# Kernel tuning notes

Hardware: AMD Instinct MI355X
Metric: run time of the kernel (lower is better)

Reference implementation:

```python
import jax, jax.numpy as jnp
import numpy as np

T = 0.1  # temperature (init arg t)


def setup_inputs() -> dict:
    key = jax.random.key(0)
    k0, k1, k2, k3 = jax.random.split(key, 4)
    B, C, H, W, N = 1, 64, 256, 256, 4096
    emb_0 = jax.random.normal(k0, (B, C, H, W), dtype=jnp.float32)
    emb_1 = jax.random.normal(k1, (B, C, H, W), dtype=jnp.float32)
    # module assumes embeddings are already L2-normalized along channels
    emb_0 = emb_0 / jnp.linalg.norm(emb_0, axis=1, keepdims=True)
    emb_1 = emb_1 / jnp.linalg.norm(emb_1, axis=1, keepdims=True)
    locations_0 = jax.random.randint(k2, (B, N, 2), 0, H).astype(jnp.float32)
    locations_1 = jax.random.randint(k3, (B, N, 2), 0, H).astype(jnp.float32)
    return {"emb_0": emb_0, "emb_1": emb_1,
            "locations_0": locations_0, "locations_1": locations_1}


def reference(emb_0, emb_1, locations_0, locations_1):
    b, c, H, W = emb_0.shape  # b == 1
    n = locations_0.shape[1]
    v = H * W
    # (b, v, c)
    e0 = emb_0.reshape(b, c, v).transpose(0, 2, 1)
    e1 = emb_1.reshape(b, c, v).transpose(0, 2, 1)
    # flatten 2D coords to linear indices: strides [W, 1]
    ind_kernel = jnp.array([W, 1], dtype=jnp.float32)
    ind_0 = (jnp.floor(locations_0) @ ind_kernel).astype(jnp.int32)[0]  # (n,)
    ind_1 = (jnp.floor(locations_1) @ ind_kernel).astype(jnp.int32)[0]  # (n,)
    e0 = e0[:, ind_0, :]  # (b, n, c)
    e1 = e1[:, ind_1, :]  # (b, n, c)
    emb = jnp.concatenate([e0, e1], axis=1)  # (b, 2n, c)
    sim = jnp.einsum('bic,bjc->bij', emb, emb)  # (b, 2n, 2n)
    exp = jnp.exp(sim / T)
    sum_e = jnp.sum(exp, axis=2) - np.exp(1.0 / T)  # subtract self-similarity
    u = jnp.arange(n)
    w = u + n
    e_uv = exp[:, u, w]  # (b, n) positive pairs
    loss = -jnp.sum(jnp.log(e_uv / sum_e[:, u]) + jnp.log(e_uv / sum_e[:, w]))
    return loss / (2 * n)
```

## Files before the change

kernel.cpp:

```cpp
#include <hip/hip_runtime.h>
#include <math.h>

#define HW2     65536
#define NLOC    4096
#define NROW    8192
#define CDIM    64
#define TINV    10.0f
#define EXP10   22026.465794806718f
#define NP      64
#define NPAIR   2080

#if __has_builtin(__builtin_amdgcn_exp2f)
#define ASCALE  14.426950408889634f
#define EXPFN(x) __builtin_amdgcn_exp2f(x)
#else
#define ASCALE  10.0f
#define EXPFN(x) __expf(x)
#endif

typedef __attribute__((ext_vector_type(8))) short bf16x8;
typedef __attribute__((ext_vector_type(4))) float f32x4;
typedef unsigned short u16;

__device__ __forceinline__ unsigned short f2bf(float f) {
  unsigned u = __builtin_bit_cast(unsigned, f);
  u += 0x7FFFu + ((u >> 16) & 1u);
  return (unsigned short)(u >> 16);
}
__device__ __forceinline__ float bf2f(unsigned u16v) {
  unsigned u = u16v << 16;
  return __builtin_bit_cast(float, u);
}

__global__ __launch_bounds__(256) void tgather_kernel(
    const float* __restrict__ emb0, const float* __restrict__ emb1,
    const float* __restrict__ loc0, const float* __restrict__ loc1,
    u16* __restrict__ Ga, u16* __restrict__ Gb) {
  __shared__ u16 T[64 * 72];
  __shared__ unsigned list[NLOC];
  __shared__ unsigned nE;

  const int tid = threadIdx.x;
  const int win = blockIdx.x;
  const int eb  = blockIdx.y;
  const float* emb = eb ? emb1 : emb0;
  const float* loc = eb ? loc1 : loc0;
  const int w0 = win * 64;

  if (tid == 0) nE = 0;

#pragma unroll
  for (int q = 0; q < 4; ++q) {
    const int c = q * 16 + (tid >> 4);
    const int x = tid & 15;
    float4 v = *reinterpret_cast<const float4*>(&emb[(size_t)c * HW2 + w0 + x * 4]);
    T[(x * 4 + 0) * 72 + c] = f2bf(v.x);
    T[(x * 4 + 1) * 72 + c] = f2bf(v.y);
    T[(x * 4 + 2) * 72 + c] = f2bf(v.z);
    T[(x * 4 + 3) * 72 + c] = f2bf(v.w);
  }
  __syncthreads();

  for (int it = tid; it < NLOC; it += 256) {
    float2 lv = *reinterpret_cast<const float2*>(&loc[it * 2]);
    int ind = (int)floorf(lv.x) * 256 + (int)floorf(lv.y);
    if ((ind >> 6) == win) {
      unsigned slot = atomicAdd(&nE, 1u);
      list[slot] = ((unsigned)it << 6) | (unsigned)(ind & 63);
    }
  }
  __syncthreads();

  const int n = (int)nE;
  const int ibase = eb * NLOC;
  const int c8 = tid & 7;
  for (int s = (tid >> 3); s < n; s += 32) {
    const unsigned ent = list[s];
    const int i = (int)(ent >> 6) + ibase;
    const int w = (int)(ent & 63u);
    bf16x8 v = *reinterpret_cast<const bf16x8*>(&T[w * 72 + c8 * 8]);
    *reinterpret_cast<bf16x8*>(&Gb[(size_t)i * CDIM + c8 * 8]) = v;
    bf16x8 vs;
#pragma unroll
    for (int j = 0; j < 8; ++j) {
      float f = bf2f((unsigned short)v[j]);
      vs[j] = (short)f2bf(f * ASCALE);
    }
    *reinterpret_cast<bf16x8*>(&Ga[(size_t)i * CDIM + c8 * 8]) = vs;
  }
}

__global__ __launch_bounds__(256) void gather_kernel(
    const float* __restrict__ emb0, const float* __restrict__ emb1,
    const float* __restrict__ loc0, const float* __restrict__ loc1,
    u16* __restrict__ Ga, u16* __restrict__ Gb) {
  int t = blockIdx.x * 256 + threadIdx.x;
  int i = t >> 6;
  int c = t & 63;
  const float* loc = (i < NLOC) ? loc0 : loc1;
  const float* emb = (i < NLOC) ? emb0 : emb1;
  int u = (i < NLOC) ? i : (i - NLOC);
  int ind = (int)floorf(loc[u * 2]) * 256 + (int)floorf(loc[u * 2 + 1]);
  float v = emb[(size_t)c * HW2 + ind];
  Gb[t] = f2bf(v);
  Ga[t] = f2bf(v * ASCALE);
}

__device__ __forceinline__ void stage_tile(u16* Bs, const u16* __restrict__ Gb,
                                           int jb, int buf, int tid, int wave,
                                           int srow, int ssl) {
#pragma unroll
  for (int r = 0; r < 2; ++r) {
    const u16* src = Gb + (size_t)(jb + r * 32 + srow) * CDIM + ssl * 8;
#if __has_builtin(__builtin_amdgcn_global_load_lds)
    u16* dst = Bs + buf * 4096 + r * 2048 + wave * 512;
    __builtin_amdgcn_global_load_lds(
        (const __attribute__((address_space(1))) unsigned int*)src,
        (__attribute__((address_space(3))) unsigned int*)dst, 16, 0, 0);
#else
    bf16x8 tmp = *reinterpret_cast<const bf16x8*>(src);
    *reinterpret_cast<bf16x8*>(Bs + buf * 4096 + r * 2048 + tid * 8) = tmp;
#endif
  }
}

__global__ __launch_bounds__(256) void simsum_tri_kernel(
    const u16* __restrict__ Ga, const u16* __restrict__ Gb,
    float* __restrict__ rowPart) {
  __shared__ u16 Bs[2 * 64 * CDIM];
  __shared__ float colRed[4][128];

  const int tid  = threadIdx.x;
  const int lane = tid & 63;
  const int wave = tid >> 6;
  const int lrow = lane & 15;
  const int kh   = lane >> 4;

  const int b = blockIdx.x;
  int p = (int)((129.0f - sqrtf(16641.0f - 8.0f * (float)b)) * 0.5f);
  if (p < 0) p = 0;
  if (p > NP - 1) p = NP - 1;
#pragma unroll
  for (int it = 0; it < 3; ++it) {
    if (p > 0 && (p * NP - p * (p - 1) / 2) > b) --p;
    else if (((p + 1) * NP - (p + 1) * p / 2) <= b) ++p;
  }
  const int q  = p + (b - (p * NP - p * (p - 1) / 2));
  const int p0 = p * 128, q0 = q * 128;
  const int i0 = p0 + wave * 32;

  const bf16x8* arowA =
      reinterpret_cast<const bf16x8*>(Ga + (size_t)(i0 + lrow) * CDIM + kh * 8);
  const bf16x8* arowB =
      reinterpret_cast<const bf16x8*>(Ga + (size_t)(i0 + 16 + lrow) * CDIM + kh * 8);
  bf16x8 aA0 = arowA[0], aA1 = arowA[4];
  bf16x8 aB0 = arowB[0], aB1 = arowB[4];

  const int srow = tid >> 3;
  const int ssl  = (tid & 7) ^ (srow & 7);
  stage_tile(Bs, Gb, q0,      0, tid, wave, srow, ssl);
  stage_tile(Bs, Gb, q0 + 64, 1, tid, wave, srow, ssl);
  __syncthreads();

  const int sp0 = ((kh ^ (lrow & 7)) << 3);
  const int sp1 = (((4 + kh) ^ (lrow & 7)) << 3);

  float accA[4][4], accB[4][4];
#pragma unroll
  for (int nf = 0; nf < 4; ++nf)
#pragma unroll
    for (int r = 0; r < 4; ++r) { accA[nf][r] = 0.f; accB[nf][r] = 0.f; }
  float colAcc[2][4];

#pragma unroll
  for (int t = 0; t < 2; ++t) {
    const u16* bs = Bs + t * 4096;
#pragma unroll
    for (int nf = 0; nf < 4; ++nf) {
      const int rb = (nf * 16 + lrow) * CDIM;
      bf16x8 b0 = *reinterpret_cast<const bf16x8*>(bs + rb + sp0);
      bf16x8 b1 = *reinterpret_cast<const bf16x8*>(bs + rb + sp1);
      f32x4 z = {0.f, 0.f, 0.f, 0.f};
      f32x4 tA = __builtin_amdgcn_mfma_f32_16x16x32_bf16(aA0, b0, z, 0, 0, 0);
      tA = __builtin_amdgcn_mfma_f32_16x16x32_bf16(aA1, b1, tA, 0, 0, 0);
      f32x4 tB = __builtin_amdgcn_mfma_f32_16x16x32_bf16(aB0, b0, z, 0, 0, 0);
      tB = __builtin_amdgcn_mfma_f32_16x16x32_bf16(aB1, b1, tB, 0, 0, 0);
      float cp = 0.f;
#pragma unroll
      for (int r = 0; r < 4; ++r) {
        float eA = EXPFN(tA[r]);
        float eB = EXPFN(tB[r]);
        accA[nf][r] += eA;
        accB[nf][r] += eB;
        cp += eA + eB;
      }
      colAcc[t][nf] = cp;
    }
  }

#pragma unroll
  for (int r = 0; r < 4; ++r) {
    float vA = (accA[0][r] + accA[1][r]) + (accA[2][r] + accA[3][r]);
    float vB = (accB[0][r] + accB[1][r]) + (accB[2][r] + accB[3][r]);
    vA += __shfl_xor(vA, 1, 16);
    vA += __shfl_xor(vA, 2, 16);
    vA += __shfl_xor(vA, 4, 16);
    vA += __shfl_xor(vA, 8, 16);
    vB += __shfl_xor(vB, 1, 16);
    vB += __shfl_xor(vB, 2, 16);
    vB += __shfl_xor(vB, 4, 16);
    vB += __shfl_xor(vB, 8, 16);
    if (lrow == 0) {
      rowPart[(size_t)(i0 + kh * 4 + r) * NP + q] = vA;
      rowPart[(size_t)(i0 + 16 + kh * 4 + r) * NP + q] = vB;
    }
  }

  if (p != q) {
#pragma unroll
    for (int t = 0; t < 2; ++t)
#pragma unroll
      for (int nf = 0; nf < 4; ++nf) {
        float c = colAcc[t][nf];
        c += __shfl_xor(c, 16, 64);
        c += __shfl_xor(c, 32, 64);
        if (kh == 0) colRed[wave][t * 64 + nf * 16 + lrow] = c;
      }
    __syncthreads();
    if (tid < 128) {
      float s = (colRed[0][tid] + colRed[1][tid]) +
                (colRed[2][tid] + colRed[3][tid]);
      rowPart[(size_t)(q0 + tid) * NP + p] = s;
    }
  }
}

__global__ __launch_bounds__(256) void finpart_kernel(
    const u16* __restrict__ Gb, const float* __restrict__ rowPart,
    float* __restrict__ partA, float* __restrict__ partB) {
  __shared__ float sA[256];
  __shared__ float sB[256];
  const int tid = threadIdx.x, b = blockIdx.x;

  float logAcc = 0.f;
  if (tid < 128) {
    const int row = b * 128 + tid;
    const float4* rp = reinterpret_cast<const float4*>(rowPart + (size_t)row * NP);
    float s = 0.f;
#pragma unroll
    for (int c = 0; c < NP / 4; ++c) {
      float4 v = rp[c];
      s += (v.x + v.y) + (v.z + v.w);
    }
    logAcc = logf(s - EXP10);
  }
  float cross = 0.f;
  if (tid < 64) {
    const int u = b * 64 + tid;
    const unsigned* r0 = reinterpret_cast<const unsigned*>(Gb + (size_t)u * CDIM);
    const unsigned* r1 =
        reinterpret_cast<const unsigned*>(Gb + (size_t)(u + NLOC) * CDIM);
#pragma unroll
    for (int c = 0; c < 32; ++c) {
      unsigned a = r0[c], bb = r1[c];
      cross += bf2f(a & 0xffffu) * bf2f(bb & 0xffffu) + bf2f(a >> 16) * bf2f(bb >> 16);
    }
  }
  sA[tid] = logAcc;
  sB[tid] = cross;
  __syncthreads();
  for (int s = 128; s > 0; s >>= 1) {
    if (tid < s) { sA[tid] += sA[tid + s]; sB[tid] += sB[tid + s]; }
    __syncthreads();
  }
  if (tid == 0) { partA[b] = sA[0]; partB[b] = sB[0]; }
}

__global__ __launch_bounds__(64) void fin2_kernel(
    const float* __restrict__ partA, const float* __restrict__ partB,
    float* __restrict__ out) {
  const int l = threadIdx.x;
  float a = partA[l];
  float c = partB[l];
#pragma unroll
  for (int s = 1; s < 64; s <<= 1) {
    a += __shfl_xor(a, s, 64);
    c += __shfl_xor(c, s, 64);
  }
  if (l == 0) out[0] = (a - 2.0f * TINV * c) / (float)NROW;
}

extern "C" void kernel_launch(void* const* d_in, const int* in_sizes, int n_in,
                              void* d_out, int out_size, void* d_ws, size_t ws_size,
                              hipStream_t stream) {
  const float* emb0 = (const float*)d_in[0];
  const float* emb1 = (const float*)d_in[1];
  const float* loc0 = (const float*)d_in[2];
  const float* loc1 = (const float*)d_in[3];
  float* out = (float*)d_out;
  char* ws = (char*)d_ws;

  u16* Ga        = (u16*)ws;
  u16* Gb        = (u16*)(ws + (1ull << 20));
  float* rowPart = (float*)(ws + (2ull << 20));
  float* partA   = (float*)(ws + (4ull << 20));
  float* partB   = partA + 64;

  dim3 tg(HW2 / 64, 2);
  tgather_kernel<<<tg, 256, 0, stream>>>(emb0, emb1, loc0, loc1, Ga, Gb);

  simsum_tri_kernel<<<NPAIR, 256, 0, stream>>>(Ga, Gb, rowPart);
  finpart_kernel<<<64, 256, 0, stream>>>(Gb, rowPart, partA, partB);
  fin2_kernel<<<1, 64, 0, stream>>>(partA, partB, out);
}
```

Before: 41.46 us.

## Replace full-tensor transpose gather with direct point gather and fuse final reduction

The gather stage no longer streams the whole embedding tensors through shared memory. Instead each block reads only the sampled locations for a 16-channel group, stages them in shared memory, and writes coalesced bf16 rows. This is meant to cut the bulk DRAM traffic of reading both full embeddings. The final two-level reduction is folded into finpart using an atomic counter and a last-block pattern, which removes one kernel launch. The trade-off is scattered, sector-granular reads and a little atomic/fence overhead.

```diff
diff --git a/kernel.cpp b/kernel.cpp
--- a/kernel.cpp
+++ b/kernel.cpp
@@ -32,78 +32,55 @@
   return __builtin_bit_cast(float, u);
 }
 
-__global__ __launch_bounds__(256) void tgather_kernel(
+__global__ __launch_bounds__(256) void gatherc_kernel(
     const float* __restrict__ emb0, const float* __restrict__ emb1,
     const float* __restrict__ loc0, const float* __restrict__ loc1,
-    u16* __restrict__ Ga, u16* __restrict__ Gb) {
-  __shared__ u16 T[64 * 72];
-  __shared__ unsigned list[NLOC];
-  __shared__ unsigned nE;
-
-  const int tid = threadIdx.x;
-  const int win = blockIdx.x;
-  const int eb  = blockIdx.y;
+    u16* __restrict__ Ga, u16* __restrict__ Gb, unsigned* __restrict__ counter) {
+  __shared__ int ind[64];
+  __shared__ u16 Gs[64][18];
+
+  const int tid   = threadIdx.x;
+  const int chunk = blockIdx.x;
+  const int cg    = blockIdx.y;
+  const int eb    = chunk >> 6;
   const float* emb = eb ? emb1 : emb0;
   const float* loc = eb ? loc1 : loc0;
-  const int w0 = win * 64;
-
-  if (tid == 0) nE = 0;
-
-#pragma unroll
-  for (int q = 0; q < 4; ++q) {
-    const int c = q * 16 + (tid >> 4);
-    const int x = tid & 15;
-    float4 v = *reinterpret_cast<const float4*>(&emb[(size_t)c * HW2 + w0 + x * 4]);
-    T[(x * 4 + 0) * 72 + c] = f2bf(v.x);
-    T[(x * 4 + 1) * 72 + c] = f2bf(v.y);
-    T[(x * 4 + 2) * 72 + c] = f2bf(v.z);
-    T[(x * 4 + 3) * 72 + c] = f2bf(v.w);
-  }
-  __syncthreads();
-
-  for (int it = tid; it < NLOC; it += 256) {
-    float2 lv = *reinterpret_cast<const float2*>(&loc[it * 2]);
-    int ind = (int)floorf(lv.x) * 256 + (int)floorf(lv.y);
-    if ((ind >> 6) == win) {
-      unsigned slot = atomicAdd(&nE, 1u);
-      list[slot] = ((unsigned)it << 6) | (unsigned)(ind & 63);
-    }
-  }
-  __syncthreads();
-
-  const int n = (int)nE;
-  const int ibase = eb * NLOC;
-  const int c8 = tid & 7;
-  for (int s = (tid >> 3); s < n; s += 32) {
-    const unsigned ent = list[s];
-    const int i = (int)(ent >> 6) + ibase;
-    const int w = (int)(ent & 63u);
-    bf16x8 v = *reinterpret_cast<const bf16x8*>(&T[w * 72 + c8 * 8]);
-    *reinterpret_cast<bf16x8*>(&Gb[(size_t)i * CDIM + c8 * 8]) = v;
+
+  if (chunk == 0 && cg == 0 && tid == 0) *counter = 0u;
+
+  if (tid < 64) {
+    const int u = (chunk & 63) * 64 + tid;
+    float2 lv = *reinterpret_cast<const float2*>(&loc[u * 2]);
+    ind[tid] = (int)floorf(lv.x) * 256 + (int)floorf(lv.y);
+  }
+  __syncthreads();
+
+  const int row = tid & 63;
+  const int cq  = tid >> 6;
+  const int pos = ind[row];
+#pragma unroll
+  for (int k = 0; k < 4; ++k) {
+    const int cl = cq + 4 * k;
+    float v = emb[(size_t)(cg * 16 + cl) * HW2 + pos];
+    Gs[row][cl] = f2bf(v);
+  }
+  __syncthreads();
+
+  const int t  = tid & 127;
+  const int r2 = t >> 1, h = t & 1;
+  const size_t gi = (size_t)(chunk * 64 + r2) * CDIM + cg * 16 + h * 8;
+  bf16x8 v = *reinterpret_cast<const bf16x8*>(&Gs[r2][h * 8]);
+  if (tid < 128) {
+    *reinterpret_cast<bf16x8*>(&Gb[gi]) = v;
+  } else {
     bf16x8 vs;
 #pragma unroll
     for (int j = 0; j < 8; ++j) {
       float f = bf2f((unsigned short)v[j]);
       vs[j] = (short)f2bf(f * ASCALE);
     }
-    *reinterpret_cast<bf16x8*>(&Ga[(size_t)i * CDIM + c8 * 8]) = vs;
-  }
-}
-
-__global__ __launch_bounds__(256) void gather_kernel(
-    const float* __restrict__ emb0, const float* __restrict__ emb1,
-    const float* __restrict__ loc0, const float* __restrict__ loc1,
-    u16* __restrict__ Ga, u16* __restrict__ Gb) {
-  int t = blockIdx.x * 256 + threadIdx.x;
-  int i = t >> 6;
-  int c = t & 63;
-  const float* loc = (i < NLOC) ? loc0 : loc1;
-  const float* emb = (i < NLOC) ? emb0 : emb1;
-  int u = (i < NLOC) ? i : (i - NLOC);
-  int ind = (int)floorf(loc[u * 2]) * 256 + (int)floorf(loc[u * 2 + 1]);
-  float v = emb[(size_t)c * HW2 + ind];
-  Gb[t] = f2bf(v);
-  Ga[t] = f2bf(v * ASCALE);
+    *reinterpret_cast<bf16x8*>(&Ga[gi]) = vs;
+  }
 }
 
 __device__ __forceinline__ void stage_tile(u16* Bs, const u16* __restrict__ Gb,
@@ -237,9 +214,11 @@
 
 __global__ __launch_bounds__(256) void finpart_kernel(
     const u16* __restrict__ Gb, const float* __restrict__ rowPart,
-    float* __restrict__ partA, float* __restrict__ partB) {
+    float* __restrict__ partA, float* __restrict__ partB,
+    unsigned* __restrict__ counter, float* __restrict__ out) {
   __shared__ float sA[256];
   __shared__ float sB[256];
+  __shared__ int lastFlag;
   const int tid = threadIdx.x, b = blockIdx.x;
 
   float logAcc = 0.f;
@@ -273,21 +252,25 @@
     if (tid < s) { sA[tid] += sA[tid + s]; sB[tid] += sB[tid + s]; }
     __syncthreads();
   }
-  if (tid == 0) { partA[b] = sA[0]; partB[b] = sB[0]; }
-}
-
-__global__ __launch_bounds__(64) void fin2_kernel(
-    const float* __restrict__ partA, const float* __restrict__ partB,
-    float* __restrict__ out) {
-  const int l = threadIdx.x;
-  float a = partA[l];
-  float c = partB[l];
-#pragma unroll
-  for (int s = 1; s < 64; s <<= 1) {
-    a += __shfl_xor(a, s, 64);
-    c += __shfl_xor(c, s, 64);
-  }
-  if (l == 0) out[0] = (a - 2.0f * TINV * c) / (float)NROW;
+  if (tid == 0) {
+    __hip_atomic_store(&partA[b], sA[0], __ATOMIC_RELAXED, __HIP_MEMORY_SCOPE_AGENT);
+    __hip_atomic_store(&partB[b], sB[0], __ATOMIC_RELAXED, __HIP_MEMORY_SCOPE_AGENT);
+    __threadfence();
+    unsigned old = atomicAdd(counter, 1u);
+    lastFlag = (old == 63u) ? 1 : 0;
+  }
+  __syncthreads();
+
+  if (lastFlag && tid < 64) {
+    float a = __hip_atomic_load(&partA[tid], __ATOMIC_RELAXED, __HIP_MEMORY_SCOPE_AGENT);
+    float c = __hip_atomic_load(&partB[tid], __ATOMIC_RELAXED, __HIP_MEMORY_SCOPE_AGENT);
+#pragma unroll
+    for (int s = 1; s < 64; s <<= 1) {
+      a += __shfl_xor(a, s, 64);
+      c += __shfl_xor(c, s, 64);
+    }
+    if (tid == 0) out[0] = (a - 2.0f * TINV * c) / (float)NROW;
+  }
 }
 
 extern "C" void kernel_launch(void* const* d_in, const int* in_sizes, int n_in,
@@ -300,16 +283,15 @@
   float* out = (float*)d_out;
   char* ws = (char*)d_ws;
 
-  u16* Ga        = (u16*)ws;
-  u16* Gb        = (u16*)(ws + (1ull << 20));
-  float* rowPart = (float*)(ws + (2ull << 20));
-  float* partA   = (float*)(ws + (4ull << 20));
-  float* partB   = partA + 64;
-
-  dim3 tg(HW2 / 64, 2);
-  tgather_kernel<<<tg, 256, 0, stream>>>(emb0, emb1, loc0, loc1, Ga, Gb);
-
+  u16* Ga           = (u16*)ws;
+  u16* Gb           = (u16*)(ws + (1ull << 20));
+  float* rowPart    = (float*)(ws + (2ull << 20));
+  float* partA      = (float*)(ws + (4ull << 20));
+  float* partB      = (float*)(ws + (4ull << 20) + 256);
+  unsigned* counter = (unsigned*)(ws + (4ull << 20) + 512);
+
+  dim3 gg(128, 4);
+  gatherc_kernel<<<gg, 256, 0, stream>>>(emb0, emb1, loc0, loc1, Ga, Gb, counter);
   simsum_tri_kernel<<<NPAIR, 256, 0, stream>>>(Ga, Gb, rowPart);
-  finpart_kernel<<<64, 256, 0, stream>>>(Gb, rowPart, partA, partB);
-  fin2_kernel<<<1, 64, 0, stream>>>(partA, partB, out);
-}
+  finpart_kernel<<<64, 256, 0, stream>>>(Gb, rowPart, partA, partB, counter, out);
+}
```

Result: faster. 36.89 us (-11.0%).
